# Kernel optimization log

Hardware: AMD Instinct MI355X
Metric: run time of the kernel (lower is better)

The kernel has to match this reference:

```python
import jax, jax.numpy as jnp
import numpy as np

N_EMBD = 1024
BLOCK_SIZE = 128
HEAD_SIZE = 128
THETA = 10000.0


def setup_inputs() -> dict:
    key = jax.random.key(0)
    k1, k2, k3, k4 = jax.random.split(key, 4)
    B, T = 256, BLOCK_SIZE
    x = jax.random.normal(k1, (B, T, N_EMBD), dtype=jnp.float32)
    # nn.Linear(n_embd, head_size, bias=False) stored as [n_embd, head_size] so y = x @ W
    s = 1.0 / np.sqrt(N_EMBD)
    Wq = jax.random.normal(k2, (N_EMBD, HEAD_SIZE), dtype=jnp.float32) * s
    Wk = jax.random.normal(k3, (N_EMBD, HEAD_SIZE), dtype=jnp.float32) * s
    Wv = jax.random.normal(k4, (N_EMBD, HEAD_SIZE), dtype=jnp.float32) * s
    return {"x": x, "Wq": Wq, "Wk": Wk, "Wv": Wv}


def _rope_cos_sin(T: int, head_size: int):
    # freqs = exp(arange(0, hs, 2) * (-log(theta)/hs)); angles = outer(t, freqs)
    inv_freq = jnp.exp(jnp.arange(0, head_size, 2, dtype=jnp.float32) * (-np.log(THETA) / head_size))
    angles = jnp.arange(T, dtype=jnp.float32)[:, None] * inv_freq[None, :]  # [T, hs/2]
    return jnp.cos(angles), jnp.sin(angles)


def _apply_rope(t, cos, sin):
    # complex-view rotation on interleaved (even, odd) pairs of the last dim
    tr = t[..., 0::2]  # real parts  [B,T,hs/2]
    ti = t[..., 1::2]  # imag parts
    out_r = tr * cos - ti * sin
    out_i = tr * sin + ti * cos
    return jnp.stack([out_r, out_i], axis=-1).reshape(t.shape)


def reference(x, Wq, Wk, Wv):
    B, T, _ = x.shape
    hs = Wq.shape[1]
    q = x @ Wq  # [B,T,hs]
    k = x @ Wk
    v = x @ Wv
    cos, sin = _rope_cos_sin(T, hs)
    q = _apply_rope(q, cos, sin)
    k = _apply_rope(k, cos, sin)
    scores = jnp.einsum('btd,bsd->bts', q, k) / jnp.sqrt(jnp.asarray(hs, q.dtype))
    causal = jnp.tril(jnp.ones((T, T), dtype=bool))
    scores = jnp.where(causal[None, :, :], scores, -jnp.inf)
    att = jax.nn.softmax(scores, axis=-1)  # dropout is identity in eval
    return jnp.einsum('bts,bsd->btd', att, v)
```

## Files before the change

kernel.cpp:

```cpp
#include <hip/hip_runtime.h>
#include <math.h>

typedef __bf16 bf16x8 __attribute__((ext_vector_type(8)));
typedef float  f32x4  __attribute__((ext_vector_type(4)));
typedef unsigned short us4 __attribute__((ext_vector_type(4)));

constexpr int N_EMBD = 1024;
constexpr int T_SEQ  = 128;
constexpr int HS     = 128;
constexpr int BATCH  = 256;

__device__ __forceinline__ void async16(const void* g, void* l) {
    __builtin_amdgcn_global_load_lds(
        (const __attribute__((address_space(1))) unsigned int*)g,
        (__attribute__((address_space(3))) unsigned int*)l, 16, 0, 0);
}
__device__ __forceinline__ unsigned short bfbits(float f) {
    return __builtin_bit_cast(unsigned short, (__bf16)f);
}
__device__ __forceinline__ f32x4 zero4() {
    f32x4 z = {0.f, 0.f, 0.f, 0.f};
    return z;
}

__global__ __launch_bounds__(256) void wcast(
    const float* __restrict__ Wq, const float* __restrict__ Wk,
    const float* __restrict__ Wv, unsigned short* __restrict__ Wt)
{
    __shared__ unsigned short tile[64][130];
    const int bid = blockIdx.x;
    const int nt  = bid >> 4;
    const int k0  = (bid & 15) << 6;
    const float* src = (nt == 0) ? Wq : ((nt == 1) ? Wk : Wv);
    const int tid = threadIdx.x;
#pragma unroll
    for (int j = 0; j < 32; ++j) {
        int idx = tid + j * 256;
        int k = idx >> 7, n = idx & 127;
        tile[k][n] = bfbits(src[(size_t)(k0 + k) * HS + n]);
    }
    __syncthreads();
#pragma unroll
    for (int j = 0; j < 32; ++j) {
        int idx = tid + j * 256;
        int n = idx >> 6, kk = idx & 63;
        Wt[(size_t)(nt * 128 + n) * N_EMBD + k0 + kk] = tile[kk][n];
    }
}

__global__ __launch_bounds__(256, 2) void qkv_rope(
    const float* __restrict__ x,
    const unsigned short* __restrict__ Wt,
    unsigned short* __restrict__ qr,
    unsigned short* __restrict__ kr,
    unsigned short* __restrict__ vT)
{
    __shared__ char lds[59392];
    constexpr int AST = 0,     ASZ = 5120;
    constexpr int BST = 10240, BSZ = 24576;

    const int tid  = threadIdx.x;
    const int w    = tid >> 6;
    const int l    = tid & 63;
    const int cl   = l & 15;
    const int quad = l >> 4;
    const int bx   = blockIdx.x;
    const int b    = bx >> 1;
    const int half = bx & 1;
    const int row0 = b * 128 + half * 64;

    const int ar = tid >> 2;
    const int ac = (tid & 3) << 3;
    const float* aptr = x + (size_t)(row0 + ar) * N_EMBD + ac;
    const int brow = l >> 2;
    const int bxo  = ((l & 3) ^ (brow & 3)) << 3;

    f32x4 acc[4][6];
#pragma unroll
    for (int a = 0; a < 4; ++a)
#pragma unroll
        for (int c = 0; c < 6; ++c) acc[a][c] = zero4();

    {
#pragma unroll
        for (int jj = 0; jj < 6; ++jj) {
            int n = w * 96 + jj * 16 + brow;
            async16(Wt + (size_t)n * N_EMBD + bxo,
                    lds + BST + (w * 96 + jj * 16) * 64);
        }
        f32x4 a0 = *(const f32x4*)(aptr);
        f32x4 a1 = *(const f32x4*)(aptr + 4);
        bf16x8 aw;
        aw[0] = (__bf16)a0[0]; aw[1] = (__bf16)a0[1];
        aw[2] = (__bf16)a0[2]; aw[3] = (__bf16)a0[3];
        aw[4] = (__bf16)a1[0]; aw[5] = (__bf16)a1[1];
        aw[6] = (__bf16)a1[2]; aw[7] = (__bf16)a1[3];
        *(bf16x8*)(lds + AST + ar * 80 + (tid & 3) * 16) = aw;
        __syncthreads();
    }

    int cur = 0;
#pragma unroll 2
    for (int t = 0; t < 32; ++t) {
        const int kc = (t + 1) << 5;
        f32x4 p0, p1;
        if (t < 31) {
            p0 = *(const f32x4*)(aptr + kc);
            p1 = *(const f32x4*)(aptr + kc + 4);
#pragma unroll
            for (int jj = 0; jj < 6; ++jj) {
                int n = w * 96 + jj * 16 + brow;
                async16(Wt + (size_t)n * N_EMBD + kc + bxo,
                        lds + BST + (cur ^ 1) * BSZ + (w * 96 + jj * 16) * 64);
            }
        }
        const char* Ab = lds + AST + cur * ASZ;
        const char* Bb = lds + BST + cur * BSZ;
        bf16x8 af[4], bf[6];
#pragma unroll
        for (int rt = 0; rt < 4; ++rt)
            af[rt] = *(const bf16x8*)(Ab + (rt * 16 + cl) * 80 + quad * 16);
#pragma unroll
        for (int ct = 0; ct < 6; ++ct) {
            int n = w * 96 + ct * 16 + cl;
            bf[ct] = *(const bf16x8*)(Bb + n * 64 + ((quad ^ (n & 3)) << 4));
        }
#pragma unroll
        for (int rt = 0; rt < 4; ++rt)
#pragma unroll
            for (int ct = 0; ct < 6; ++ct)
                acc[rt][ct] = __builtin_amdgcn_mfma_f32_16x16x32_bf16(
                    af[rt], bf[ct], acc[rt][ct], 0, 0, 0);
        if (t < 31) {
            __builtin_amdgcn_sched_barrier(0);
            bf16x8 aw;
            aw[0] = (__bf16)p0[0]; aw[1] = (__bf16)p0[1];
            aw[2] = (__bf16)p0[2]; aw[3] = (__bf16)p0[3];
            aw[4] = (__bf16)p1[0]; aw[5] = (__bf16)p1[1];
            aw[6] = (__bf16)p1[2]; aw[7] = (__bf16)p1[3];
            *(bf16x8*)(lds + AST + (cur ^ 1) * ASZ + ar * 80 + (tid & 3) * 16) = aw;
        }
        __syncthreads();
        cur ^= 1;
    }

    const float LNT = 0.07195578430905272f;
#pragma unroll
    for (int ct = 0; ct < 6; ++ct) {
        int c0  = w * 96 + ct * 16;
        int ntc = c0 >> 7;
        int d   = (c0 & 127) + cl;
        if (ntc < 2) {
            unsigned short* dst = ((ntc == 0) ? qr : kr) + (size_t)b * 16384;
            float freq = __expf(-(float)(d & ~1) * LNT);
#pragma unroll
            for (int rt = 0; rt < 4; ++rt) {
#pragma unroll
                for (int i = 0; i < 4; ++i) {
                    int tt = half * 64 + rt * 16 + quad * 4 + i;
                    float v = acc[rt][ct][i];
                    float p = __shfl_xor(v, 1);
                    float sn, cs;
                    __sincosf((float)tt * freq, &sn, &cs);
                    float r = ((d & 1) == 0) ? (v * cs - p * sn) : (p * sn + v * cs);
                    dst[(size_t)tt * HS + d] = bfbits(r);
                }
            }
        } else {
#pragma unroll
            for (int rt = 0; rt < 4; ++rt) {
                int t0 = half * 64 + rt * 16 + quad * 4;
                us4 u;
                u.x = bfbits(acc[rt][ct][0]);
                u.y = bfbits(acc[rt][ct][1]);
                u.z = bfbits(acc[rt][ct][2]);
                u.w = bfbits(acc[rt][ct][3]);
                *(us4*)(vT + (size_t)b * 16384 + (size_t)d * T_SEQ + t0) = u;
            }
        }
    }
}

__global__ __launch_bounds__(256, 2) void attn(
    const unsigned short* __restrict__ qr,
    const unsigned short* __restrict__ kr,
    const unsigned short* __restrict__ vT,
    float* __restrict__ out)
{
    __shared__ char lds[17408];
    const int tid  = threadIdx.x;
    const int w    = tid >> 6;
    const int l    = tid & 63;
    const int cl   = l & 15;
    const int quad = l >> 4;
    const int bx   = blockIdx.x;
    const int b    = bx & 255;
    const int seg  = ((bx >> 8) << 2) + w;
    const int nct  = seg + 1;
    const int nks  = (seg + 2) >> 1;
    char* pl = lds + w * 4352;

    const unsigned short* qb = qr + (size_t)b * 16384;
    const unsigned short* kb = kr + (size_t)b * 16384;
    const unsigned short* vb = vT + (size_t)b * 16384;

    bf16x8 qf[4];
#pragma unroll
    for (int ks = 0; ks < 4; ++ks)
        qf[ks] = *(const bf16x8*)(qb + (seg * 16 + cl) * HS + ks * 32 + quad * 8);

    f32x4 s[8];
#pragma unroll
    for (int ct = 0; ct < 8; ++ct) s[ct] = zero4();

#pragma unroll
    for (int ct = 0; ct < 8; ++ct) if (ct < nct) {
#pragma unroll
        for (int ks = 0; ks < 4; ++ks) {
            bf16x8 kk = *(const bf16x8*)(kb + (ct * 16 + cl) * HS + ks * 32 + quad * 8);
            s[ct] = __builtin_amdgcn_mfma_f32_16x16x32_bf16(qf[ks], kk, s[ct], 0, 0, 0);
        }
    }

    const float scale = 0.08838834764831845f;
#pragma unroll
    for (int i = 0; i < 4; ++i) {
        int t = seg * 16 + quad * 4 + i;
        float mx = -3.0e38f;
#pragma unroll
        for (int ct = 0; ct < 8; ++ct) if (ct < nct) {
            int col = ct * 16 + cl;
            float v = s[ct][i] * scale;
            v = (col <= t) ? v : -INFINITY;
            s[ct][i] = v;
            mx = fmaxf(mx, v);
        }
        mx = fmaxf(mx, __shfl_xor(mx, 1));
        mx = fmaxf(mx, __shfl_xor(mx, 2));
        mx = fmaxf(mx, __shfl_xor(mx, 4));
        mx = fmaxf(mx, __shfl_xor(mx, 8));
        float sum = 0.f;
#pragma unroll
        for (int ct = 0; ct < 8; ++ct) if (ct < nct) {
            float p = __expf(s[ct][i] - mx);
            s[ct][i] = p;
            sum += p;
        }
        sum += __shfl_xor(sum, 1);
        sum += __shfl_xor(sum, 2);
        sum += __shfl_xor(sum, 4);
        sum += __shfl_xor(sum, 8);
        float inv = 1.0f / sum;
        int rl = quad * 4 + i;
#pragma unroll
        for (int ct = 0; ct < 8; ++ct) if (ct < nct) {
            *(unsigned short*)(pl + rl * 272 + (ct * 16 + cl) * 2) =
                bfbits(s[ct][i] * inv);
        }
        if ((seg & 1) == 0) {
            *(unsigned short*)(pl + rl * 272 + (nct * 16 + cl) * 2) = 0;
        }
    }

    bf16x8 ap[4];
#pragma unroll
    for (int ks = 0; ks < 4; ++ks) if (ks < nks)
        ap[ks] = *(const bf16x8*)(pl + cl * 272 + (ks * 4 + quad) * 16);

    f32x4 o[8];
#pragma unroll
    for (int ct = 0; ct < 8; ++ct) o[ct] = zero4();

#pragma unroll
    for (int ct = 0; ct < 8; ++ct) {
#pragma unroll
        for (int ks = 0; ks < 4; ++ks) if (ks < nks) {
            bf16x8 vv = *(const bf16x8*)(vb + (ct * 16 + cl) * T_SEQ + ks * 32 + quad * 8);
            o[ct] = __builtin_amdgcn_mfma_f32_16x16x32_bf16(ap[ks], vv, o[ct], 0, 0, 0);
        }
    }

#pragma unroll
    for (int ct = 0; ct < 8; ++ct)
#pragma unroll
        for (int i = 0; i < 4; ++i) {
            int t = seg * 16 + quad * 4 + i;
            out[(size_t)b * 16384 + (size_t)t * HS + ct * 16 + cl] = o[ct][i];
        }
}

extern "C" void kernel_launch(void* const* d_in, const int* in_sizes, int n_in,
                              void* d_out, int out_size, void* d_ws, size_t ws_size,
                              hipStream_t stream) {
    const float* x  = (const float*)d_in[0];
    const float* Wq = (const float*)d_in[1];
    const float* Wk = (const float*)d_in[2];
    const float* Wv = (const float*)d_in[3];
    float* out = (float*)d_out;

    char* ws = (char*)d_ws;
    unsigned short* Wt = (unsigned short*)ws;
    unsigned short* q  = (unsigned short*)(ws + (1  << 20));
    unsigned short* k  = (unsigned short*)(ws + (9  << 20));
    unsigned short* vT = (unsigned short*)(ws + (17 << 20));

    wcast<<<48, 256, 0, stream>>>(Wq, Wk, Wv, Wt);
    qkv_rope<<<512, 256, 0, stream>>>(x, Wt, q, k, vT);
    attn<<<512, 256, 0, stream>>>(q, k, vT, out);
}
```

Before: 248.1 us.

## Stream fp32 x tiles via async LDS loads with explicit waitcnt pipeline

The QKV projection mainloop now loads the fp32 x tile directly into LDS with global_load_lds, using an XOR swizzle, instead of loading into registers, converting to bf16 and storing. Conversion to bf16 moves to after the LDS read. The loop is restructured into a manually double-buffered pipeline with explicit vmcnt/lgkmcnt waits and raw s_barrier, so global loads overlap compute without register staging. In exchange the A buffer doubles in size (fp32), LDS grows to 64KB, LDS read traffic increases, and the conversion work is repeated per wave.

After: 244.4 us. Within noise of the previous version (-1.5%).

```diff
diff --git a/kernel.cpp b/kernel.cpp
--- a/kernel.cpp
+++ b/kernel.cpp
@@ -55,9 +55,9 @@
     unsigned short* __restrict__ kr,
     unsigned short* __restrict__ vT)
 {
-    __shared__ char lds[59392];
-    constexpr int AST = 0,     ASZ = 5120;
-    constexpr int BST = 10240, BSZ = 24576;
+    __shared__ char lds[65536];
+    constexpr int ASZ  = 8192;
+    constexpr int BOFF = 16384, BSZ = 24576;
 
     const int tid  = threadIdx.x;
     const int w    = tid >> 6;
@@ -69,11 +69,19 @@
     const int half = bx & 1;
     const int row0 = b * 128 + half * 64;
 
-    const int ar = tid >> 2;
-    const int ac = (tid & 3) << 3;
-    const float* aptr = x + (size_t)(row0 + ar) * N_EMBD + ac;
+    const int arj = l >> 3;
+    const int agr = (l & 7) ^ arj;
+    const float* aS0 = x + (size_t)(row0 + 16 * w + arj) * N_EMBD + agr * 4;
+    const float* aS1 = x + (size_t)(row0 + 16 * w + 8 + arj) * N_EMBD + agr * 4;
+
     const int brow = l >> 2;
     const int bxo  = ((l & 3) ^ (brow & 3)) << 3;
+    const unsigned short* bS0 = Wt + (size_t)(w * 96 +  0 + brow) * N_EMBD + bxo;
+    const unsigned short* bS1 = Wt + (size_t)(w * 96 + 16 + brow) * N_EMBD + bxo;
+    const unsigned short* bS2 = Wt + (size_t)(w * 96 + 32 + brow) * N_EMBD + bxo;
+    const unsigned short* bS3 = Wt + (size_t)(w * 96 + 48 + brow) * N_EMBD + bxo;
+    const unsigned short* bS4 = Wt + (size_t)(w * 96 + 64 + brow) * N_EMBD + bxo;
+    const unsigned short* bS5 = Wt + (size_t)(w * 96 + 80 + brow) * N_EMBD + bxo;
 
     f32x4 acc[4][6];
 #pragma unroll
@@ -81,68 +89,76 @@
 #pragma unroll
         for (int c = 0; c < 6; ++c) acc[a][c] = zero4();
 
-    {
-#pragma unroll
-        for (int jj = 0; jj < 6; ++jj) {
-            int n = w * 96 + jj * 16 + brow;
-            async16(Wt + (size_t)n * N_EMBD + bxo,
-                    lds + BST + (w * 96 + jj * 16) * 64);
-        }
-        f32x4 a0 = *(const f32x4*)(aptr);
-        f32x4 a1 = *(const f32x4*)(aptr + 4);
-        bf16x8 aw;
-        aw[0] = (__bf16)a0[0]; aw[1] = (__bf16)a0[1];
-        aw[2] = (__bf16)a0[2]; aw[3] = (__bf16)a0[3];
-        aw[4] = (__bf16)a1[0]; aw[5] = (__bf16)a1[1];
-        aw[6] = (__bf16)a1[2]; aw[7] = (__bf16)a1[3];
-        *(bf16x8*)(lds + AST + ar * 80 + (tid & 3) * 16) = aw;
-        __syncthreads();
-    }
-
-    int cur = 0;
-#pragma unroll 2
-    for (int t = 0; t < 32; ++t) {
-        const int kc = (t + 1) << 5;
-        f32x4 p0, p1;
-        if (t < 31) {
-            p0 = *(const f32x4*)(aptr + kc);
-            p1 = *(const f32x4*)(aptr + kc + 4);
-#pragma unroll
-            for (int jj = 0; jj < 6; ++jj) {
-                int n = w * 96 + jj * 16 + brow;
-                async16(Wt + (size_t)n * N_EMBD + kc + bxo,
-                        lds + BST + (cur ^ 1) * BSZ + (w * 96 + jj * 16) * 64);
-            }
-        }
-        const char* Ab = lds + AST + cur * ASZ;
-        const char* Bb = lds + BST + cur * BSZ;
-        bf16x8 af[4], bf[6];
-#pragma unroll
-        for (int rt = 0; rt < 4; ++rt)
-            af[rt] = *(const bf16x8*)(Ab + (rt * 16 + cl) * 80 + quad * 16);
-#pragma unroll
-        for (int ct = 0; ct < 6; ++ct) {
-            int n = w * 96 + ct * 16 + cl;
-            bf[ct] = *(const bf16x8*)(Bb + n * 64 + ((quad ^ (n & 3)) << 4));
-        }
-#pragma unroll
-        for (int rt = 0; rt < 4; ++rt)
-#pragma unroll
-            for (int ct = 0; ct < 6; ++ct)
-                acc[rt][ct] = __builtin_amdgcn_mfma_f32_16x16x32_bf16(
-                    af[rt], bf[ct], acc[rt][ct], 0, 0, 0);
-        if (t < 31) {
-            __builtin_amdgcn_sched_barrier(0);
-            bf16x8 aw;
-            aw[0] = (__bf16)p0[0]; aw[1] = (__bf16)p0[1];
-            aw[2] = (__bf16)p0[2]; aw[3] = (__bf16)p0[3];
-            aw[4] = (__bf16)p1[0]; aw[5] = (__bf16)p1[1];
-            aw[6] = (__bf16)p1[2]; aw[7] = (__bf16)p1[3];
-            *(bf16x8*)(lds + AST + (cur ^ 1) * ASZ + ar * 80 + (tid & 3) * 16) = aw;
-        }
-        __syncthreads();
-        cur ^= 1;
-    }
+#define STAGE(DST)                                                            \
+    __builtin_amdgcn_sched_barrier(0);                                        \
+    async16(aS0, lds + (DST) * ASZ + (2 * w + 0) * 1024);                     \
+    async16(aS1, lds + (DST) * ASZ + (2 * w + 1) * 1024);                     \
+    async16(bS0, lds + BOFF + (DST) * BSZ + (w * 96 +  0) * 64);              \
+    async16(bS1, lds + BOFF + (DST) * BSZ + (w * 96 + 16) * 64);              \
+    async16(bS2, lds + BOFF + (DST) * BSZ + (w * 96 + 32) * 64);              \
+    async16(bS3, lds + BOFF + (DST) * BSZ + (w * 96 + 48) * 64);              \
+    async16(bS4, lds + BOFF + (DST) * BSZ + (w * 96 + 64) * 64);              \
+    async16(bS5, lds + BOFF + (DST) * BSZ + (w * 96 + 80) * 64);              \
+    aS0 += 32; aS1 += 32;                                                     \
+    bS0 += 32; bS1 += 32; bS2 += 32; bS3 += 32; bS4 += 32; bS5 += 32;         \
+    __builtin_amdgcn_sched_barrier(0);
+
+#define COMPUTE(CSEL) {                                                       \
+    const char* Ab = lds + (CSEL) * ASZ;                                      \
+    const char* Bb = lds + BOFF + (CSEL) * BSZ;                               \
+    bf16x8 af[4]; bf16x8 bf[6];                                               \
+    _Pragma("unroll")                                                         \
+    for (int rt = 0; rt < 4; ++rt) {                                          \
+        int m = rt * 16 + cl;                                                 \
+        f32x4 u0 = *(const f32x4*)(Ab + m * 128 + (((quad * 2)     ^ (m & 7)) << 4)); \
+        f32x4 u1 = *(const f32x4*)(Ab + m * 128 + (((quad * 2 + 1) ^ (m & 7)) << 4)); \
+        af[rt][0] = (__bf16)u0[0]; af[rt][1] = (__bf16)u0[1];                 \
+        af[rt][2] = (__bf16)u0[2]; af[rt][3] = (__bf16)u0[3];                 \
+        af[rt][4] = (__bf16)u1[0]; af[rt][5] = (__bf16)u1[1];                 \
+        af[rt][6] = (__bf16)u1[2]; af[rt][7] = (__bf16)u1[3];                 \
+    }                                                                         \
+    _Pragma("unroll")                                                         \
+    for (int ct = 0; ct < 6; ++ct) {                                          \
+        int n = w * 96 + ct * 16 + cl;                                        \
+        bf[ct] = *(const bf16x8*)(Bb + n * 64 + ((quad ^ (n & 3)) << 4));     \
+    }                                                                         \
+    _Pragma("unroll")                                                         \
+    for (int rt = 0; rt < 4; ++rt)                                            \
+        _Pragma("unroll")                                                     \
+        for (int ct = 0; ct < 6; ++ct)                                        \
+            acc[rt][ct] = __builtin_amdgcn_mfma_f32_16x16x32_bf16(            \
+                af[rt], bf[ct], acc[rt][ct], 0, 0, 0);                        \
+}
+
+#define GSTEP(CSEL)                                                           \
+    STAGE((CSEL) ^ 1)                                                         \
+    asm volatile("s_waitcnt vmcnt(8)" ::: "memory");                          \
+    __builtin_amdgcn_sched_barrier(0);                                        \
+    __builtin_amdgcn_s_barrier();                                             \
+    __builtin_amdgcn_sched_barrier(0);                                        \
+    COMPUTE(CSEL)                                                             \
+    __builtin_amdgcn_sched_barrier(0);                                        \
+    asm volatile("s_waitcnt lgkmcnt(0)" ::: "memory");                        \
+    __builtin_amdgcn_s_barrier();
+
+    STAGE(0)
+
+    for (int t = 0; t < 30; t += 2) {
+        GSTEP(0)
+        GSTEP(1)
+    }
+    GSTEP(0)
+
+    __builtin_amdgcn_sched_barrier(0);
+    asm volatile("s_waitcnt vmcnt(0)" ::: "memory");
+    __builtin_amdgcn_sched_barrier(0);
+    __builtin_amdgcn_s_barrier();
+    __builtin_amdgcn_sched_barrier(0);
+    COMPUTE(1)
+
+#undef STAGE
+#undef COMPUTE
+#undef GSTEP
 
     const float LNT = 0.07195578430905272f;
 #pragma unroll
```

## Shrink QKV GEMM tile to 32 rows, single-buffer LDS, async-load fp32 A

Applied to the files above, without the earlier changes.

The QKV projection kernel now processes 32 rows per block instead of 64, launching 1024 blocks. It drops LDS double buffering, which lets occupancy rise to 4 blocks per CU. The fp32 activation tile is now streamed straight into LDS with async global-to-LDS loads and converted to bf16 when read into registers, using an XOR-swizzled layout, where before it went through registers and was converted before the LDS store. This trades overlap of loads with compute (two barriers per k-step, no prefetch) and more redundant reads of the weight matrix for higher occupancy and less register pressure.

Result: slower. 276.9 us (+11.6%).

```diff
diff --git a/kernel.cpp b/kernel.cpp
--- a/kernel.cpp
+++ b/kernel.cpp
@@ -48,16 +48,15 @@
     }
 }
 
-__global__ __launch_bounds__(256, 2) void qkv_rope(
+__global__ __launch_bounds__(256, 4) void qkv_rope(
     const float* __restrict__ x,
     const unsigned short* __restrict__ Wt,
     unsigned short* __restrict__ qr,
     unsigned short* __restrict__ kr,
     unsigned short* __restrict__ vT)
 {
-    __shared__ char lds[59392];
-    constexpr int AST = 0,     ASZ = 5120;
-    constexpr int BST = 10240, BSZ = 24576;
+    __shared__ char lds[28672];
+    constexpr int BOFF = 4096;
 
     const int tid  = threadIdx.x;
     const int w    = tid >> 6;
@@ -65,83 +64,75 @@
     const int cl   = l & 15;
     const int quad = l >> 4;
     const int bx   = blockIdx.x;
-    const int b    = bx >> 1;
-    const int half = bx & 1;
-    const int row0 = b * 128 + half * 64;
-
-    const int ar = tid >> 2;
-    const int ac = (tid & 3) << 3;
-    const float* aptr = x + (size_t)(row0 + ar) * N_EMBD + ac;
+    const int b    = bx >> 2;
+    const int quarter = bx & 3;
+    const int row0 = b * 128 + quarter * 32;
+
+    const int arj = l >> 3;
+    const int agr = (l & 7) ^ arj;
+    const float* aS0 = x + (size_t)(row0 + 8 * w + arj) * N_EMBD + agr * 4;
+
     const int brow = l >> 2;
     const int bxo  = ((l & 3) ^ (brow & 3)) << 3;
-
-    f32x4 acc[4][6];
-#pragma unroll
-    for (int a = 0; a < 4; ++a)
+    const unsigned short* bS0 = Wt + (size_t)(w * 96 +  0 + brow) * N_EMBD + bxo;
+    const unsigned short* bS1 = Wt + (size_t)(w * 96 + 16 + brow) * N_EMBD + bxo;
+    const unsigned short* bS2 = Wt + (size_t)(w * 96 + 32 + brow) * N_EMBD + bxo;
+    const unsigned short* bS3 = Wt + (size_t)(w * 96 + 48 + brow) * N_EMBD + bxo;
+    const unsigned short* bS4 = Wt + (size_t)(w * 96 + 64 + brow) * N_EMBD + bxo;
+    const unsigned short* bS5 = Wt + (size_t)(w * 96 + 80 + brow) * N_EMBD + bxo;
+
+    f32x4 acc[2][6];
+#pragma unroll
+    for (int a = 0; a < 2; ++a)
 #pragma unroll
         for (int c = 0; c < 6; ++c) acc[a][c] = zero4();
 
-    {
-#pragma unroll
-        for (int jj = 0; jj < 6; ++jj) {
-            int n = w * 96 + jj * 16 + brow;
-            async16(Wt + (size_t)n * N_EMBD + bxo,
-                    lds + BST + (w * 96 + jj * 16) * 64);
-        }
-        f32x4 a0 = *(const f32x4*)(aptr);
-        f32x4 a1 = *(const f32x4*)(aptr + 4);
-        bf16x8 aw;
-        aw[0] = (__bf16)a0[0]; aw[1] = (__bf16)a0[1];
-        aw[2] = (__bf16)a0[2]; aw[3] = (__bf16)a0[3];
-        aw[4] = (__bf16)a1[0]; aw[5] = (__bf16)a1[1];
-        aw[6] = (__bf16)a1[2]; aw[7] = (__bf16)a1[3];
-        *(bf16x8*)(lds + AST + ar * 80 + (tid & 3) * 16) = aw;
+    async16(aS0, lds + w * 1024);
+    async16(bS0, lds + BOFF + (w * 96 +  0) * 64);
+    async16(bS1, lds + BOFF + (w * 96 + 16) * 64);
+    async16(bS2, lds + BOFF + (w * 96 + 32) * 64);
+    async16(bS3, lds + BOFF + (w * 96 + 48) * 64);
+    async16(bS4, lds + BOFF + (w * 96 + 64) * 64);
+    async16(bS5, lds + BOFF + (w * 96 + 80) * 64);
+    aS0 += 32;
+    bS0 += 32; bS1 += 32; bS2 += 32; bS3 += 32; bS4 += 32; bS5 += 32;
+
+    for (int t = 0; t < 32; ++t) {
         __syncthreads();
-    }
-
-    int cur = 0;
-#pragma unroll 2
-    for (int t = 0; t < 32; ++t) {
-        const int kc = (t + 1) << 5;
-        f32x4 p0, p1;
-        if (t < 31) {
-            p0 = *(const f32x4*)(aptr + kc);
-            p1 = *(const f32x4*)(aptr + kc + 4);
-#pragma unroll
-            for (int jj = 0; jj < 6; ++jj) {
-                int n = w * 96 + jj * 16 + brow;
-                async16(Wt + (size_t)n * N_EMBD + kc + bxo,
-                        lds + BST + (cur ^ 1) * BSZ + (w * 96 + jj * 16) * 64);
-            }
-        }
-        const char* Ab = lds + AST + cur * ASZ;
-        const char* Bb = lds + BST + cur * BSZ;
-        bf16x8 af[4], bf[6];
-#pragma unroll
-        for (int rt = 0; rt < 4; ++rt)
-            af[rt] = *(const bf16x8*)(Ab + (rt * 16 + cl) * 80 + quad * 16);
+        bf16x8 af[2], bf[6];
+#pragma unroll
+        for (int rt = 0; rt < 2; ++rt) {
+            int m = rt * 16 + cl;
+            f32x4 u0 = *(const f32x4*)(lds + m * 128 + (((quad * 2)     ^ (m & 7)) << 4));
+            f32x4 u1 = *(const f32x4*)(lds + m * 128 + (((quad * 2 + 1) ^ (m & 7)) << 4));
+            af[rt][0] = (__bf16)u0[0]; af[rt][1] = (__bf16)u0[1];
+            af[rt][2] = (__bf16)u0[2]; af[rt][3] = (__bf16)u0[3];
+            af[rt][4] = (__bf16)u1[0]; af[rt][5] = (__bf16)u1[1];
+            af[rt][6] = (__bf16)u1[2]; af[rt][7] = (__bf16)u1[3];
+        }
 #pragma unroll
         for (int ct = 0; ct < 6; ++ct) {
             int n = w * 96 + ct * 16 + cl;
-            bf[ct] = *(const bf16x8*)(Bb + n * 64 + ((quad ^ (n & 3)) << 4));
-        }
-#pragma unroll
-        for (int rt = 0; rt < 4; ++rt)
+            bf[ct] = *(const bf16x8*)(lds + BOFF + n * 64 + ((quad ^ (n & 3)) << 4));
+        }
+#pragma unroll
+        for (int rt = 0; rt < 2; ++rt)
 #pragma unroll
             for (int ct = 0; ct < 6; ++ct)
                 acc[rt][ct] = __builtin_amdgcn_mfma_f32_16x16x32_bf16(
                     af[rt], bf[ct], acc[rt][ct], 0, 0, 0);
+        __syncthreads();
         if (t < 31) {
-            __builtin_amdgcn_sched_barrier(0);
-            bf16x8 aw;
-            aw[0] = (__bf16)p0[0]; aw[1] = (__bf16)p0[1];
-            aw[2] = (__bf16)p0[2]; aw[3] = (__bf16)p0[3];
-            aw[4] = (__bf16)p1[0]; aw[5] = (__bf16)p1[1];
-            aw[6] = (__bf16)p1[2]; aw[7] = (__bf16)p1[3];
-            *(bf16x8*)(lds + AST + (cur ^ 1) * ASZ + ar * 80 + (tid & 3) * 16) = aw;
-        }
-        __syncthreads();
-        cur ^= 1;
+            async16(aS0, lds + w * 1024);
+            async16(bS0, lds + BOFF + (w * 96 +  0) * 64);
+            async16(bS1, lds + BOFF + (w * 96 + 16) * 64);
+            async16(bS2, lds + BOFF + (w * 96 + 32) * 64);
+            async16(bS3, lds + BOFF + (w * 96 + 48) * 64);
+            async16(bS4, lds + BOFF + (w * 96 + 64) * 64);
+            async16(bS5, lds + BOFF + (w * 96 + 80) * 64);
+            aS0 += 32;
+            bS0 += 32; bS1 += 32; bS2 += 32; bS3 += 32; bS4 += 32; bS5 += 32;
+        }
     }
 
     const float LNT = 0.07195578430905272f;
@@ -154,10 +145,10 @@
             unsigned short* dst = ((ntc == 0) ? qr : kr) + (size_t)b * 16384;
             float freq = __expf(-(float)(d & ~1) * LNT);
 #pragma unroll
-            for (int rt = 0; rt < 4; ++rt) {
+            for (int rt = 0; rt < 2; ++rt) {
 #pragma unroll
                 for (int i = 0; i < 4; ++i) {
-                    int tt = half * 64 + rt * 16 + quad * 4 + i;
+                    int tt = quarter * 32 + rt * 16 + quad * 4 + i;
                     float v = acc[rt][ct][i];
                     float p = __shfl_xor(v, 1);
                     float sn, cs;
@@ -168,8 +159,8 @@
             }
         } else {
 #pragma unroll
-            for (int rt = 0; rt < 4; ++rt) {
-                int t0 = half * 64 + rt * 16 + quad * 4;
+            for (int rt = 0; rt < 2; ++rt) {
+                int t0 = quarter * 32 + rt * 16 + quad * 4;
                 us4 u;
                 u.x = bfbits(acc[rt][ct][0]);
                 u.y = bfbits(acc[rt][ct][1]);
@@ -305,6 +296,6 @@
     unsigned short* vT = (unsigned short*)(ws + (17 << 20));
 
     wcast<<<48, 256, 0, stream>>>(Wq, Wk, Wv, Wt);
-    qkv_rope<<<512, 256, 0, stream>>>(x, Wt, q, k, vT);
+    qkv_rope<<<1024, 256, 0, stream>>>(x, Wt, q, k, vT);
     attn<<<512, 256, 0, stream>>>(q, k, vT, out);
 }
```

## Read weight fragments directly from global memory instead of staging in LDS

Applied to the files above, without the earlier changes.

The QKV projection kernel no longer copies the transposed bf16 weight tile into a double-buffered LDS region with async global-to-LDS loads. Each wave now loads its B-operand MFMA fragments straight from global memory, relying on cache hits since the weights are small and shared by all blocks. This shrinks the kernel's LDS footprint, so the launch bound goes from 2 to 3 blocks per SM for more latency hiding. The cost is that weight loads are no longer prefetched one step ahead: each iteration issues strided global reads right before its MFMAs. The loop unroll pragma and the scheduling barrier are also removed.

Measured after the change: 267.8 us. 1.08x slower.

```diff
diff --git a/kernel.cpp b/kernel.cpp
--- a/kernel.cpp
+++ b/kernel.cpp
@@ -10,11 +10,6 @@
 constexpr int HS     = 128;
 constexpr int BATCH  = 256;
 
-__device__ __forceinline__ void async16(const void* g, void* l) {
-    __builtin_amdgcn_global_load_lds(
-        (const __attribute__((address_space(1))) unsigned int*)g,
-        (__attribute__((address_space(3))) unsigned int*)l, 16, 0, 0);
-}
 __device__ __forceinline__ unsigned short bfbits(float f) {
     return __builtin_bit_cast(unsigned short, (__bf16)f);
 }
@@ -48,16 +43,15 @@
     }
 }
 
-__global__ __launch_bounds__(256, 2) void qkv_rope(
+__global__ __launch_bounds__(256, 3) void qkv_rope(
     const float* __restrict__ x,
     const unsigned short* __restrict__ Wt,
     unsigned short* __restrict__ qr,
     unsigned short* __restrict__ kr,
     unsigned short* __restrict__ vT)
 {
-    __shared__ char lds[59392];
-    constexpr int AST = 0,     ASZ = 5120;
-    constexpr int BST = 10240, BSZ = 24576;
+    __shared__ char lds[20480];
+    constexpr int ASZ = 10240;
 
     const int tid  = threadIdx.x;
     const int w    = tid >> 6;
@@ -72,8 +66,6 @@
     const int ar = tid >> 2;
     const int ac = (tid & 3) << 3;
     const float* aptr = x + (size_t)(row0 + ar) * N_EMBD + ac;
-    const int brow = l >> 2;
-    const int bxo  = ((l & 3) ^ (brow & 3)) << 3;
 
     f32x4 acc[4][6];
 #pragma unroll
@@ -82,12 +74,6 @@
         for (int c = 0; c < 6; ++c) acc[a][c] = zero4();
 
     {
-#pragma unroll
-        for (int jj = 0; jj < 6; ++jj) {
-            int n = w * 96 + jj * 16 + brow;
-            async16(Wt + (size_t)n * N_EMBD + bxo,
-                    lds + BST + (w * 96 + jj * 16) * 64);
-        }
         f32x4 a0 = *(const f32x4*)(aptr);
         f32x4 a1 = *(const f32x4*)(aptr + 4);
         bf16x8 aw;
@@ -95,36 +81,27 @@
         aw[2] = (__bf16)a0[2]; aw[3] = (__bf16)a0[3];
         aw[4] = (__bf16)a1[0]; aw[5] = (__bf16)a1[1];
         aw[6] = (__bf16)a1[2]; aw[7] = (__bf16)a1[3];
-        *(bf16x8*)(lds + AST + ar * 80 + (tid & 3) * 16) = aw;
+        *(bf16x8*)(lds + ar * 80 + (tid & 3) * 16) = aw;
         __syncthreads();
     }
 
     int cur = 0;
-#pragma unroll 2
     for (int t = 0; t < 32; ++t) {
-        const int kc = (t + 1) << 5;
         f32x4 p0, p1;
         if (t < 31) {
-            p0 = *(const f32x4*)(aptr + kc);
-            p1 = *(const f32x4*)(aptr + kc + 4);
-#pragma unroll
-            for (int jj = 0; jj < 6; ++jj) {
-                int n = w * 96 + jj * 16 + brow;
-                async16(Wt + (size_t)n * N_EMBD + kc + bxo,
-                        lds + BST + (cur ^ 1) * BSZ + (w * 96 + jj * 16) * 64);
-            }
-        }
-        const char* Ab = lds + AST + cur * ASZ;
-        const char* Bb = lds + BST + cur * BSZ;
-        bf16x8 af[4], bf[6];
-#pragma unroll
-        for (int rt = 0; rt < 4; ++rt)
-            af[rt] = *(const bf16x8*)(Ab + (rt * 16 + cl) * 80 + quad * 16);
+            p0 = *(const f32x4*)(aptr + (t + 1) * 32);
+            p1 = *(const f32x4*)(aptr + (t + 1) * 32 + 4);
+        }
+        bf16x8 bf[6];
 #pragma unroll
         for (int ct = 0; ct < 6; ++ct) {
             int n = w * 96 + ct * 16 + cl;
-            bf[ct] = *(const bf16x8*)(Bb + n * 64 + ((quad ^ (n & 3)) << 4));
-        }
+            bf[ct] = *(const bf16x8*)(Wt + (size_t)n * N_EMBD + t * 32 + quad * 8);
+        }
+        bf16x8 af[4];
+#pragma unroll
+        for (int rt = 0; rt < 4; ++rt)
+            af[rt] = *(const bf16x8*)(lds + cur * ASZ + (rt * 16 + cl) * 80 + quad * 16);
 #pragma unroll
         for (int rt = 0; rt < 4; ++rt)
 #pragma unroll
@@ -132,13 +109,12 @@
                 acc[rt][ct] = __builtin_amdgcn_mfma_f32_16x16x32_bf16(
                     af[rt], bf[ct], acc[rt][ct], 0, 0, 0);
         if (t < 31) {
-            __builtin_amdgcn_sched_barrier(0);
             bf16x8 aw;
             aw[0] = (__bf16)p0[0]; aw[1] = (__bf16)p0[1];
             aw[2] = (__bf16)p0[2]; aw[3] = (__bf16)p0[3];
             aw[4] = (__bf16)p1[0]; aw[5] = (__bf16)p1[1];
             aw[6] = (__bf16)p1[2]; aw[7] = (__bf16)p1[3];
-            *(bf16x8*)(lds + AST + (cur ^ 1) * ASZ + ar * 80 + (tid & 3) * 16) = aw;
+            *(bf16x8*)(lds + (cur ^ 1) * ASZ + ar * 80 + (tid & 3) * 16) = aw;
         }
         __syncthreads();
         cur ^= 1;
```
